# Performance work log

Hardware: AMD Instinct MI355X
Metric: run time of the kernel (lower is better)

The kernel has to match this reference:

```python
import jax, jax.numpy as jnp
import numpy as np

PH, PW = 7, 7            # output_size
SCALE = 0.25             # spatial_scale
SR = 2                   # sampling_ratio (fixed, jit-static)
ALIGNED = True


def setup_inputs() -> dict:
    key = jax.random.key(0)
    k1, k2, k3, k4, k5 = jax.random.split(key, 5)
    B, C, H, W = 4, 256, 200, 200
    N = 512
    img = H / SCALE  # 800.0 image size
    x = jax.random.normal(k1, (B, C, H, W), dtype=jnp.float32)
    bidx = jax.random.randint(k2, (N,), 0, B).astype(jnp.float32)
    cxy = jax.random.uniform(k3, (N, 2), minval=0.0, maxval=img)
    wh = jax.random.uniform(k4, (N, 2), minval=32.0, maxval=256.0)
    x1y1 = jnp.clip(cxy - wh / 2, 0.0, img - 1.0)
    x2y2 = jnp.clip(cxy + wh / 2, 0.0, img - 1.0)
    rois = jnp.concatenate([bidx[:, None], x1y1[:, 0:1], x1y1[:, 1:2],
                            x2y2[:, 0:1], x2y2[:, 1:2]], axis=1).astype(jnp.float32)
    return {"input": x, "rois": rois}


def _axis_samples(start, bin_size, P, size):
    """Sample coords along one axis. start/bin_size: [N]. Returns per-sample
    low/high integer indices, interp weights, and validity mask, all [N, P*SR]."""
    ib = jnp.arange(P, dtype=jnp.float32)           # bin index
    isr = jnp.arange(SR, dtype=jnp.float32)         # sample within bin
    # coord[n, p, s] = start + p*bin + (s+0.5)*bin/SR
    coord = (start[:, None, None]
             + ib[None, :, None] * bin_size[:, None, None]
             + (isr[None, None, :] + 0.5) * bin_size[:, None, None] / SR)
    coord = coord.reshape(coord.shape[0], P * SR)
    valid = (coord >= -1.0) & (coord <= size)
    c = jnp.maximum(coord, 0.0)
    lo_raw = jnp.floor(c).astype(jnp.int32)
    at_edge = lo_raw >= size - 1
    lo = jnp.where(at_edge, size - 1, lo_raw)
    hi = jnp.where(at_edge, size - 1, lo_raw + 1)
    cv = jnp.where(at_edge, jnp.float32(size - 1), c)
    frac = cv - lo.astype(jnp.float32)              # weight toward hi
    return lo, hi, frac, valid


def reference(input, rois):
    B, C, H, W = input.shape
    N = rois.shape[0]
    b = rois[:, 0].astype(jnp.int32)
    off = 0.5 if ALIGNED else 0.0
    sx = rois[:, 1] * SCALE - off
    sy = rois[:, 2] * SCALE - off
    ex = rois[:, 3] * SCALE - off
    ey = rois[:, 4] * SCALE - off
    rw, rh = ex - sx, ey - sy
    if not ALIGNED:
        rw = jnp.maximum(rw, 1.0)
        rh = jnp.maximum(rh, 1.0)
    bin_w, bin_h = rw / PW, rh / PH

    yl, yh, fy, vy = _axis_samples(sy, bin_h, PH, H)   # [N, Sy]
    xl, xh, fx, vx = _axis_samples(sx, bin_w, PW, W)   # [N, Sx]

    featT = jnp.transpose(input, (0, 2, 3, 1))         # [B,H,W,C]

    def gather(yi, xi):  # -> [N, Sy, Sx, C]
        return featT[b[:, None, None], yi[:, :, None], xi[:, None, :]]

    hy, ly = (1.0 - fy), fy
    hx, lx = (1.0 - fx), fx
    w_ll = (hy[:, :, None] * hx[:, None, :])[..., None]
    w_lh = (hy[:, :, None] * lx[:, None, :])[..., None]
    w_hl = (ly[:, :, None] * hx[:, None, :])[..., None]
    w_hh = (ly[:, :, None] * lx[:, None, :])[..., None]

    val = (w_ll * gather(yl, xl) + w_lh * gather(yl, xh)
           + w_hl * gather(yh, xl) + w_hh * gather(yh, xh))
    mask = (vy[:, :, None] & vx[:, None, :])[..., None]
    val = jnp.where(mask, val, 0.0)                    # [N, Sy, Sx, C]

    # average pool the SRxSR samples per output bin
    val = val.reshape(N, PH, SR, PW, SR, C).mean(axis=(2, 4))  # [N,PH,PW,C]
    return jnp.transpose(val, (0, 3, 1, 2))            # [N,C,PH,PW]
```

## Files before the change

### kernel.cpp

```cpp
#include <hip/hip_runtime.h>


#define R_PH 7
#define R_PW 7
#define R_SR 2
#define R_SCALE 0.25f
#define R_C 256
#define R_H 200
#define R_W 200
#define R_HW (R_H * R_W)
#define STRIP 25
#define NSTRIP 8
#define NLISTS 32
#define STAGE_ROWS 31

__device__ __forceinline__ void axis_sample(float start, float bin, int p, int s, int size,
                                            int& lo, int& hi, float& wlo, float& whi) {
    float coord = (start + (float)p * bin) + ((float)s + 0.5f) * bin * (1.0f / R_SR);
    bool valid = (coord >= -1.0f) && (coord <= (float)size);
    float c = fmaxf(coord, 0.0f);
    int lo_raw = (int)floorf(c);
    bool at_edge = lo_raw >= size - 1;
    lo = at_edge ? size - 1 : lo_raw;
    hi = at_edge ? size - 1 : lo_raw + 1;
    float cv = at_edge ? (float)(size - 1) : c;
    float frac = cv - (float)lo;
    whi = valid ? frac : 0.0f;
    wlo = valid ? (1.0f - frac) : 0.0f;
}

__global__ void __launch_bounds__(512)
build_lists(const float* __restrict__ rois, int N, int* __restrict__ ws) {
    __shared__ int lcnt[NLISTS];
    int t = threadIdx.x;
    if (t < NLISTS) lcnt[t] = 0;
    __syncthreads();
    int*    lists = ws + NLISTS;
    int4*   yrows = (int4*)(lists + NLISTS * N * R_PH);
    float4* yw    = (float4*)(yrows + N * R_PH);
    int4*   xcols = (int4*)(yw + N * R_PH);
    float4* xw    = (float4*)(xcols + N * R_PH);

    for (int n = t; n < N; n += 512) {
        const float* r = rois + (size_t)n * 5;
        int b = (int)r[0];
        float sx = r[1] * R_SCALE - 0.5f;
        float sy = r[2] * R_SCALE - 0.5f;
        float ex = r[3] * R_SCALE - 0.5f;
        float ey = r[4] * R_SCALE - 0.5f;
        float binw = (ex - sx) * (1.0f / R_PW);
        float binh = (ey - sy) * (1.0f / R_PH);
        for (int p = 0; p < R_PH; ++p) {
            int lo0, hi0, lo1, hi1; float wl0, wh0, wl1, wh1;
            axis_sample(sy, binh, p, 0, R_H, lo0, hi0, wl0, wh0);
            axis_sample(sy, binh, p, 1, R_H, lo1, hi1, wl1, wh1);
            yrows[n * R_PH + p] = make_int4(lo0 * R_W, hi0 * R_W, lo1 * R_W, hi1 * R_W);
            yw[n * R_PH + p]    = make_float4(wl0 * 0.25f, wh0 * 0.25f, wl1 * 0.25f, wh1 * 0.25f);
            int bs = b * NSTRIP + lo0 / STRIP;
            int pos = atomicAdd(&lcnt[bs], 1);
            lists[bs * (N * R_PH) + pos] = (n << 3) | p;
            axis_sample(sx, binw, p, 0, R_W, lo0, hi0, wl0, wh0);
            axis_sample(sx, binw, p, 1, R_W, lo1, hi1, wl1, wh1);
            xcols[n * R_PH + p] = make_int4(lo0, hi0, lo1, hi1);
            xw[n * R_PH + p]    = make_float4(wl0, wh0, wl1, wh1);
        }
    }
    __syncthreads();
    if (t < NLISTS) ws[t] = lcnt[t];
}

__global__ void __launch_bounds__(512)
roi_strip(const float* __restrict__ input,
          const int* __restrict__ ws, int N,
          float* __restrict__ out) {
    __shared__ float pl[STAGE_ROWS * R_W];
    int c = blockIdx.x;
    int b = blockIdx.y;
    int s = blockIdx.z;
    int r0 = s * STRIP;
    int nrows = min(STAGE_ROWS, R_H - r0);

    const float4* src = (const float4*)(input + (size_t)(b * R_C + c) * R_HW + r0 * R_W);
    float4* dstv = (float4*)pl;
    int nf4 = nrows * (R_W / 4);
    for (int i = threadIdx.x; i < nf4; i += 512) dstv[i] = src[i];

    int m = ws[b * NSTRIP + s];
    const int*    lists = ws + NLISTS;
    const int*    list  = lists + (b * NSTRIP + s) * (N * R_PH);
    const int4*   yrows = (const int4*)(lists + NLISTS * N * R_PH);
    const float4* yw    = (const float4*)(yrows + N * R_PH);
    const int4*   xcols = (const int4*)(yw + N * R_PH);
    const float4* xw    = (const float4*)(xcols + N * R_PH);
    __syncthreads();

    int r0b = r0 * R_W;
    int total = m * R_PW;
    for (int i = threadIdx.x; i < total; i += 512) {
        int e  = i / R_PW;
        int pw = i - e * R_PW;
        int code = list[e];
        int n  = code >> 3;
        int ph = code & 7;
        int4   yr  = yrows[n * R_PH + ph];
        float4 ywt = yw[n * R_PH + ph];
        int4   xc  = xcols[n * R_PH + pw];
        float4 xwt = xw[n * R_PH + pw];

        const float* p0 = pl + (yr.x - r0b);
        const float* p1 = pl + (yr.y - r0b);
        const float* p2 = pl + (yr.z - r0b);
        const float* p3 = pl + (yr.w - r0b);
        float s0 = xwt.x * p0[xc.x] + xwt.y * p0[xc.y] + xwt.z * p0[xc.z] + xwt.w * p0[xc.w];
        float s1 = xwt.x * p1[xc.x] + xwt.y * p1[xc.y] + xwt.z * p1[xc.z] + xwt.w * p1[xc.w];
        float s2 = xwt.x * p2[xc.x] + xwt.y * p2[xc.y] + xwt.z * p2[xc.z] + xwt.w * p2[xc.w];
        float s3 = xwt.x * p3[xc.x] + xwt.y * p3[xc.y] + xwt.z * p3[xc.z] + xwt.w * p3[xc.w];
        out[(size_t)(n * R_C + c) * 49 + ph * R_PW + pw] =
            ywt.x * s0 + ywt.y * s1 + ywt.z * s2 + ywt.w * s3;
    }
}

__global__ void __launch_bounds__(256)
roi_align_fwd(const float* __restrict__ input,
              const float* __restrict__ rois,
              float* __restrict__ out, int total) {
    int idx = blockIdx.x * blockDim.x + threadIdx.x;
    if (idx >= total) return;
    int pw = idx % R_PW;
    int ph = (idx / R_PW) % R_PH;
    int c  = (idx / (R_PW * R_PH)) % R_C;
    int n  = idx / (R_PW * R_PH * R_C);
    const float* r = rois + (size_t)n * 5;
    int   b  = (int)r[0];
    float sx = r[1] * R_SCALE - 0.5f;
    float sy = r[2] * R_SCALE - 0.5f;
    float ex = r[3] * R_SCALE - 0.5f;
    float ey = r[4] * R_SCALE - 0.5f;
    float bin_w = (ex - sx) * (1.0f / R_PW);
    float bin_h = (ey - sy) * (1.0f / R_PH);
    const float* plane = input + (size_t)(b * R_C + c) * R_HW;
    int   ylo[R_SR], yhi[R_SR], xlo[R_SR], xhi[R_SR];
    float wylo[R_SR], wyhi[R_SR], wxlo[R_SR], wxhi[R_SR];
#pragma unroll
    for (int s = 0; s < R_SR; ++s) {
        axis_sample(sy, bin_h, ph, s, R_H, ylo[s], yhi[s], wylo[s], wyhi[s]);
        axis_sample(sx, bin_w, pw, s, R_W, xlo[s], xhi[s], wxlo[s], wxhi[s]);
    }
    float acc = 0.0f;
#pragma unroll
    for (int ys = 0; ys < R_SR; ++ys) {
        const float* row_lo = plane + ylo[ys] * R_W;
        const float* row_hi = plane + yhi[ys] * R_W;
#pragma unroll
        for (int xs = 0; xs < R_SR; ++xs) {
            acc += wylo[ys] * (wxlo[xs] * row_lo[xlo[xs]] + wxhi[xs] * row_lo[xhi[xs]])
                 + wyhi[ys] * (wxlo[xs] * row_hi[xlo[xs]] + wxhi[xs] * row_hi[xhi[xs]]);
        }
    }
    out[idx] = acc * (1.0f / (R_SR * R_SR));
}

extern "C" void kernel_launch(void* const* d_in, const int* in_sizes, int n_in,
                              void* d_out, int out_size, void* d_ws, size_t ws_size,
                              hipStream_t stream) {
    const float* input = (const float*)d_in[0];
    const float* rois  = (const float*)d_in[1];
    float* out = (float*)d_out;
    int N = in_sizes[1] / 5;

    size_t ws_needed = (size_t)(NLISTS + NLISTS * N * R_PH + 16 * N * R_PH) * sizeof(int);
    if (ws_size >= ws_needed) {
        int* ws = (int*)d_ws;
        build_lists<<<1, 512, 0, stream>>>(rois, N, ws);
        dim3 grid(R_C, 4, NSTRIP);
        roi_strip<<<grid, 512, 0, stream>>>(input, ws, N, out);
    } else {
        int total = out_size;
        roi_align_fwd<<<(total + 255) / 256, 256, 0, stream>>>(input, rois, out, total);
    }
}
```

Before: 275.2 us.

## Use larger strips, direct global-to-LDS staging, and prefetch per-item ROI metadata

Halves the number of row strips per plane (50 rows staged, 56-row halo), so each plane is loaded fewer times with less halo overlap. Staging switches from register float4 copies to the global_load_lds builtin, and each thread's first work item's metadata is loaded before the barrier, with the next item prefetched inside the loop. The aim is to overlap the input plane load with metadata latency and to cut redundant halo traffic. The trade-offs are about 45 KB of LDS per block, which limits occupancy, and fewer blocks overall.

```diff
diff --git a/kernel.cpp b/kernel.cpp
--- a/kernel.cpp
+++ b/kernel.cpp
@@ -9,10 +9,10 @@
 #define R_H 200
 #define R_W 200
 #define R_HW (R_H * R_W)
-#define STRIP 25
-#define NSTRIP 8
-#define NLISTS 32
-#define STAGE_ROWS 31
+#define STRIP 50
+#define NSTRIP 4
+#define NLISTS 16
+#define STAGE_ROWS 56
 
 __device__ __forceinline__ void axis_sample(float start, float bin, int p, int s, int size,
                                             int& lo, int& hi, float& wlo, float& whi) {
@@ -69,7 +69,7 @@
     if (t < NLISTS) ws[t] = lcnt[t];
 }
 
-__global__ void __launch_bounds__(512)
+__global__ void __launch_bounds__(512, 6)
 roi_strip(const float* __restrict__ input,
           const int* __restrict__ ws, int N,
           float* __restrict__ out) {
@@ -77,13 +77,23 @@
     int c = blockIdx.x;
     int b = blockIdx.y;
     int s = blockIdx.z;
+    int t = threadIdx.x;
+    int wave = t >> 6;
+    int lane = t & 63;
     int r0 = s * STRIP;
-    int nrows = min(STAGE_ROWS, R_H - r0);
-
-    const float4* src = (const float4*)(input + (size_t)(b * R_C + c) * R_HW + r0 * R_W);
-    float4* dstv = (float4*)pl;
-    int nf4 = nrows * (R_W / 4);
-    for (int i = threadIdx.x; i < nf4; i += 512) dstv[i] = src[i];
+
+    const float* src = input + (size_t)(b * R_C + c) * R_HW + r0 * R_W;
+    int vmax = min(STAGE_ROWS, R_H - r0) * (R_W / 4);
+    for (int ch = wave; ch < (STAGE_ROWS * R_W / 4 + 63) / 64; ch += 8) {
+        int elem = ch * 64 + lane;
+        if (elem < STAGE_ROWS * R_W / 4) {
+            int ge = min(elem, vmax - 1);
+            __builtin_amdgcn_global_load_lds(
+                (const __attribute__((address_space(1))) void*)(src + ge * 4),
+                (__attribute__((address_space(3))) void*)(pl + ch * 256),
+                16, 0, 0);
+        }
+    }
 
     int m = ws[b * NSTRIP + s];
     const int*    lists = ws + NLISTS;
@@ -92,21 +102,39 @@
     const float4* yw    = (const float4*)(yrows + N * R_PH);
     const int4*   xcols = (const int4*)(yw + N * R_PH);
     const float4* xw    = (const float4*)(xcols + N * R_PH);
+
+    int total = m * R_PW;
+    int r0b = r0 * R_W;
+
+    int4 yr; float4 ywt; int4 xc; float4 xwt; size_t oidx;
+    int i = t;
+    bool have = i < total;
+    if (have) {
+        int e = i / R_PW, pw = i - e * R_PW;
+        int code = list[e];
+        int n = code >> 3, ph = code & 7;
+        yr  = yrows[n * R_PH + ph];
+        ywt = yw[n * R_PH + ph];
+        xc  = xcols[n * R_PH + pw];
+        xwt = xw[n * R_PH + pw];
+        oidx = (size_t)(n * R_C + c) * 49 + ph * R_PW + pw;
+    }
     __syncthreads();
 
-    int r0b = r0 * R_W;
-    int total = m * R_PW;
-    for (int i = threadIdx.x; i < total; i += 512) {
-        int e  = i / R_PW;
-        int pw = i - e * R_PW;
-        int code = list[e];
-        int n  = code >> 3;
-        int ph = code & 7;
-        int4   yr  = yrows[n * R_PH + ph];
-        float4 ywt = yw[n * R_PH + ph];
-        int4   xc  = xcols[n * R_PH + pw];
-        float4 xwt = xw[n * R_PH + pw];
-
+    while (have) {
+        int inext = i + 512;
+        bool hnext = inext < total;
+        int4 yr2; float4 ywt2; int4 xc2; float4 xwt2; size_t oidx2;
+        if (hnext) {
+            int e = inext / R_PW, pw = inext - e * R_PW;
+            int code = list[e];
+            int n = code >> 3, ph = code & 7;
+            yr2  = yrows[n * R_PH + ph];
+            ywt2 = yw[n * R_PH + ph];
+            xc2  = xcols[n * R_PH + pw];
+            xwt2 = xw[n * R_PH + pw];
+            oidx2 = (size_t)(n * R_C + c) * 49 + ph * R_PW + pw;
+        }
         const float* p0 = pl + (yr.x - r0b);
         const float* p1 = pl + (yr.y - r0b);
         const float* p2 = pl + (yr.z - r0b);
@@ -115,8 +143,9 @@
         float s1 = xwt.x * p1[xc.x] + xwt.y * p1[xc.y] + xwt.z * p1[xc.z] + xwt.w * p1[xc.w];
         float s2 = xwt.x * p2[xc.x] + xwt.y * p2[xc.y] + xwt.z * p2[xc.z] + xwt.w * p2[xc.w];
         float s3 = xwt.x * p3[xc.x] + xwt.y * p3[xc.y] + xwt.z * p3[xc.z] + xwt.w * p3[xc.w];
-        out[(size_t)(n * R_C + c) * 49 + ph * R_PW + pw] =
-            ywt.x * s0 + ywt.y * s1 + ywt.z * s2 + ywt.w * s3;
+        out[oidx] = ywt.x * s0 + ywt.y * s1 + ywt.z * s2 + ywt.w * s3;
+        yr = yr2; ywt = ywt2; xc = xc2; xwt = xwt2; oidx = oidx2;
+        i = inext; have = hnext;
     }
 }
 
```

Result: faster. 263.7 us (-4.2%).
